# Kernel optimization log

Measured on AMD Instinct MI355X. Metric: run time of the kernel, lower is better.

Reference implementation:

```python
import jax, jax.numpy as jnp
import numpy as np

TAU = 0.07
COS_EPS = 1e-8   # torch F.cosine_similarity eps
L1_EPS = 1e-12   # torch F.normalize eps
MM_EPS = 1e-8    # min-max renorm eps

B, C, H, W = 64, 256, 32, 32
S, D = 512, 256


def setup_inputs() -> dict:
    key = jax.random.key(0)
    k1, k2, k3, k4 = jax.random.split(key, 4)
    scale = 1.0 / np.sqrt(D)
    return {
        "image_patches": jax.random.normal(k1, (B, C, H, W), dtype=jnp.float32),
        "text_tokens": jax.random.normal(k2, (B, S, D), dtype=jnp.float32),
        "Wv": jax.random.normal(k3, (D, D), dtype=jnp.float32) * scale,
        "bv": jnp.zeros((D,), dtype=jnp.float32),
        "Wt": jax.random.normal(k4, (D, D), dtype=jnp.float32) * scale,
        "bt": jnp.zeros((D,), dtype=jnp.float32),
    }


def _linear(x, Wgt, b):
    return x @ Wgt.T + b


def _l2n(x, axis=-1):
    n = jnp.maximum(jnp.linalg.norm(x, axis=axis, keepdims=True), COS_EPS)
    return x / n


def _sym_ce_diag(sim):
    # sim [..., N, N]; mean of -log_softmax diagonals along both class axes
    lsm_r = jax.nn.log_softmax(sim, axis=-1)
    lsm_c = jax.nn.log_softmax(sim, axis=-2)
    d_r = jnp.diagonal(lsm_r, axis1=-2, axis2=-1)
    d_c = jnp.diagonal(lsm_c, axis1=-2, axis2=-1)
    return 0.5 * (-jnp.mean(d_r) - jnp.mean(d_c))


def reference(image_patches, text_tokens, Wv, bv, Wt, bt):
    b, c, h, w = image_patches.shape
    hw = h * w
    # b c h w -> b (h w) c, then adapters
    patches = image_patches.reshape(b, c, hw).transpose(0, 2, 1)  # [b, hw, c]
    patches = _linear(patches, Wv, bv)          # [b, hw, d]
    tokens = _linear(text_tokens, Wt, bt)       # [b, s, d]

    # global embeddings: mean-pool then adapter (adapter applied twice on vision path)
    g_img = _linear(jnp.mean(patches, axis=1), Wv, bv)  # [b, d]
    g_txt = _linear(jnp.mean(tokens, axis=1), Wt, bt)   # [b, d]

    # global contrastive loss (cosine sim / tau, symmetric CE over batch)
    g_sim = (_l2n(g_img) @ _l2n(g_txt).T) / TAU         # [b, b]
    global_loss = _sym_ce_diag(g_sim)

    # fine-grained alignment
    sim = jnp.einsum('bpd,bsd->bps', patches, tokens)   # [b, hw, s]
    mn = jnp.min(sim, axis=1, keepdims=True)
    mx = jnp.max(sim, axis=1, keepdims=True)
    sim = (sim - mn) / (mx - mn + MM_EPS)
    sigma = 1.0 / hw
    sim = jnp.where(sim < sigma, 0.0, sim)
    # L1 normalize over patch dim (torch F.normalize p=1 dim=1)
    weights = sim / jnp.maximum(jnp.sum(jnp.abs(sim), axis=1, keepdims=True), L1_EPS)
    lgve = jnp.einsum('bps,bpd->bsd', weights, patches)  # [b, s, d]

    # fine-grained contrastive loss: cosine sim between grouped-vision and text tokens
    f_sim = jnp.einsum('bid,bjd->bij', _l2n(lgve), _l2n(tokens)) / TAU  # [b, s, s]
    fine_loss = _sym_ce_diag(f_sim)

    return global_loss + fine_loss
```

## Files before the change

kernel.cpp:

```cpp
#include <hip/hip_runtime.h>
#include <math.h>

#define BB   64
#define HWP  1024
#define SS   512
#define DD   256
#define TAU_INV (1.0f/0.07f)
#define SIGMA   (1.0f/1024.0f)

typedef unsigned short us;
typedef __attribute__((ext_vector_type(8))) short short8v;
typedef __attribute__((ext_vector_type(8))) unsigned short ushort8v;
typedef __attribute__((ext_vector_type(4))) float floatx4;

__device__ __forceinline__ float bf2f(us u) {
    return __uint_as_float((unsigned)u << 16);
}
__device__ __forceinline__ us f2bf(float f) {
    unsigned u = __float_as_uint(f);
    u += 0x7FFFu + ((u >> 16) & 1u);
    return (us)(u >> 16);
}
__device__ __forceinline__ void split_bf(float v, us& h, us& l) {
    h = f2bf(v);
    l = f2bf(v - bf2f(h));
}

__global__ void zero_out_k(float* out) { if (threadIdx.x == 0) out[0] = 0.0f; }

enum { OPM_F32_ROW = 0, OPM_F32_COL = 1, OPM_SPL_ROW = 2, OPM_SPL_COL = 3,
       OPM_B16_COL = 4, OPM_B16_ROW = 5, OPM_WGT_COL = 6 };
enum { OUT_F32 = 0, OUT_B16 = 1 };

#define LDSTRIDE 40

template<int MODE, int ROWS, int NW>
struct SRegs {
    static constexpr int RR = ROWS / 128;
    static constexpr bool ISF32 = (MODE == OPM_F32_ROW) || (MODE == OPM_F32_COL);
    ushort8v h[ISF32 ? 1 : RR][2];
    ushort8v l[(MODE == OPM_SPL_ROW) ? RR : 1][2];
    float4   f[ISF32 ? RR : 1][4];
};

template<int MODE, int ROWS, int NW>
__device__ __forceinline__ void stage_load(
    const char* p0, const char* p1, int ld, int row0, int k0, int tid,
    SRegs<MODE, ROWS, NW>& R)
{
    #pragma unroll
    for (int rr = 0; rr < ROWS / 128; ++rr) {
        if constexpr (MODE == OPM_SPL_ROW) {
            const us* ph = (const us*)p0;
            const us* pl = (const us*)p1;
            const int i = rr * 128 + (tid >> 1), ko = (tid & 1) * 16;
            const long long g = (long long)(row0 + i) * ld + k0 + ko;
            R.h[rr][0] = *(const ushort8v*)&ph[g];
            R.h[rr][1] = *(const ushort8v*)&ph[g + 8];
            R.l[rr][0] = *(const ushort8v*)&pl[g];
            R.l[rr][1] = *(const ushort8v*)&pl[g + 8];
        } else if constexpr (MODE == OPM_B16_ROW) {
            const us* ph = (const us*)p0;
            if constexpr (NW == 4) {
                const int i = rr * 128 + (tid >> 1), ko = (tid & 1) * 16;
                const long long g = (long long)(row0 + i) * ld + k0 + ko;
                R.h[rr][0] = *(const ushort8v*)&ph[g];
                R.h[rr][1] = *(const ushort8v*)&ph[g + 8];
            } else {
                const int i = rr * 128 + (tid >> 2), ko = (tid & 3) * 8;
                const long long g = (long long)(row0 + i) * ld + k0 + ko;
                R.h[rr][0] = *(const ushort8v*)&ph[g];
            }
        } else if constexpr (MODE == OPM_F32_ROW) {
            const float* pf = (const float*)p0;
            const int i = rr * 128 + (tid >> 1), ko = (tid & 1) * 16;
            const long long g = (long long)(row0 + i) * ld + k0 + ko;
            #pragma unroll
            for (int c = 0; c < 4; ++c)
                R.f[rr][c] = *(const float4*)&pf[g + c * 4];
        } else if constexpr (MODE == OPM_F32_COL) {
            const float* pf = (const float*)p0;
            const int m = rr * 128 + (tid & 127), kh = (tid >> 7) * 16;
            const long long base = (long long)(k0 + kh) * ld + row0 + m;
            #pragma unroll
            for (int c = 0; c < 4; ++c) {
                float4 v;
                v.x = pf[base + (long long)(c * 4 + 0) * ld];
                v.y = pf[base + (long long)(c * 4 + 1) * ld];
                v.z = pf[base + (long long)(c * 4 + 2) * ld];
                v.w = pf[base + (long long)(c * 4 + 3) * ld];
                R.f[rr][c] = v;
            }
        } else {
            const us* ph = (const us*)p0;
            if constexpr (NW == 4) {
                const int m = rr * 128 + (tid & 127), kh = (tid >> 7) * 16;
                const long long base = (long long)(k0 + kh) * ld + row0 + m;
                #pragma unroll
                for (int kk = 0; kk < 8; ++kk) {
                    R.h[rr][0][kk] = ph[base + (long long)kk * ld];
                    R.h[rr][1][kk] = ph[base + (long long)(kk + 8) * ld];
                }
            } else {
                const int m = rr * 128 + (tid & 127), kh = (tid >> 7) * 8;
                const long long base = (long long)(k0 + kh) * ld + row0 + m;
                #pragma unroll
                for (int kk = 0; kk < 8; ++kk)
                    R.h[rr][0][kk] = ph[base + (long long)kk * ld];
            }
        }
    }
}

template<int MODE, int ROWS, int NW>
__device__ __forceinline__ void stage_store(
    const SRegs<MODE, ROWS, NW>& R, us* ldsH, us* ldsL, int tid, float nlo, float inv)
{
    #pragma unroll
    for (int rr = 0; rr < ROWS / 128; ++rr) {
        if constexpr (MODE == OPM_SPL_ROW) {
            const int i = rr * 128 + (tid >> 1), ko = (tid & 1) * 16;
            *(ushort8v*)&ldsH[i * LDSTRIDE + ko]     = R.h[rr][0];
            *(ushort8v*)&ldsH[i * LDSTRIDE + ko + 8] = R.h[rr][1];
            *(ushort8v*)&ldsL[i * LDSTRIDE + ko]     = R.l[rr][0];
            *(ushort8v*)&ldsL[i * LDSTRIDE + ko + 8] = R.l[rr][1];
        } else if constexpr (MODE == OPM_B16_ROW) {
            if constexpr (NW == 4) {
                const int i = rr * 128 + (tid >> 1), ko = (tid & 1) * 16;
                *(ushort8v*)&ldsH[i * LDSTRIDE + ko]     = R.h[rr][0];
                *(ushort8v*)&ldsH[i * LDSTRIDE + ko + 8] = R.h[rr][1];
            } else {
                const int i = rr * 128 + (tid >> 2), ko = (tid & 3) * 8;
                *(ushort8v*)&ldsH[i * LDSTRIDE + ko] = R.h[rr][0];
            }
        } else if constexpr (MODE == OPM_F32_ROW) {
            const int i = rr * 128 + (tid >> 1), ko = (tid & 1) * 16;
            us h16[16], l16a[16];
            #pragma unroll
            for (int c = 0; c < 4; ++c) {
                float4 v = R.f[rr][c];
                split_bf(v.x, h16[c*4+0], l16a[c*4+0]);
                split_bf(v.y, h16[c*4+1], l16a[c*4+1]);
                split_bf(v.z, h16[c*4+2], l16a[c*4+2]);
                split_bf(v.w, h16[c*4+3], l16a[c*4+3]);
            }
            *(ushort8v*)&ldsH[i * LDSTRIDE + ko]     = *(const ushort8v*)&h16[0];
            *(ushort8v*)&ldsH[i * LDSTRIDE + ko + 8] = *(const ushort8v*)&h16[8];
            *(ushort8v*)&ldsL[i * LDSTRIDE + ko]     = *(const ushort8v*)&l16a[0];
            *(ushort8v*)&ldsL[i * LDSTRIDE + ko + 8] = *(const ushort8v*)&l16a[8];
        } else if constexpr (MODE == OPM_F32_COL) {
            const int m = rr * 128 + (tid & 127), kh = (tid >> 7) * 16;
            us vh[16], vl[16];
            #pragma unroll
            for (int c = 0; c < 4; ++c) {
                float4 v = R.f[rr][c];
                split_bf(v.x, vh[c*4+0], vl[c*4+0]);
                split_bf(v.y, vh[c*4+1], vl[c*4+1]);
                split_bf(v.z, vh[c*4+2], vl[c*4+2]);
                split_bf(v.w, vh[c*4+3], vl[c*4+3]);
            }
            *(ushort8v*)&ldsH[m * LDSTRIDE + kh]     = *(const ushort8v*)&vh[0];
            *(ushort8v*)&ldsH[m * LDSTRIDE + kh + 8] = *(const ushort8v*)&vh[8];
            *(ushort8v*)&ldsL[m * LDSTRIDE + kh]     = *(const ushort8v*)&vl[0];
            *(ushort8v*)&ldsL[m * LDSTRIDE + kh + 8] = *(const ushort8v*)&vl[8];
        } else if constexpr (MODE == OPM_B16_COL) {
            if constexpr (NW == 4) {
                const int m = rr * 128 + (tid & 127), kh = (tid >> 7) * 16;
                *(ushort8v*)&ldsH[m * LDSTRIDE + kh]     = R.h[rr][0];
                *(ushort8v*)&ldsH[m * LDSTRIDE + kh + 8] = R.h[rr][1];
            } else {
                const int m = rr * 128 + (tid & 127), kh = (tid >> 7) * 8;
                *(ushort8v*)&ldsH[m * LDSTRIDE + kh] = R.h[rr][0];
            }
        } else if constexpr (MODE == OPM_WGT_COL) {
            if constexpr (NW == 4) {
                const int m = rr * 128 + (tid & 127), kh = (tid >> 7) * 16;
                us v[16];
                #pragma unroll
                for (int kk = 0; kk < 8; ++kk) {
                    const float w0 = fmaf(bf2f(R.h[rr][0][kk]), inv, nlo);
                    const float w1 = fmaf(bf2f(R.h[rr][1][kk]), inv, nlo);
                    v[kk]     = (w0 < SIGMA) ? (us)0 : f2bf(w0);
                    v[kk + 8] = (w1 < SIGMA) ? (us)0 : f2bf(w1);
                }
                *(ushort8v*)&ldsH[m * LDSTRIDE + kh]     = *(const ushort8v*)&v[0];
                *(ushort8v*)&ldsH[m * LDSTRIDE + kh + 8] = *(const ushort8v*)&v[8];
            } else {
                const int m = rr * 128 + (tid & 127), kh = (tid >> 7) * 8;
                us v[8];
                #pragma unroll
                for (int kk = 0; kk < 8; ++kk) {
                    const float w0 = fmaf(bf2f(R.h[rr][0][kk]), inv, nlo);
                    v[kk] = (w0 < SIGMA) ? (us)0 : f2bf(w0);
                }
                *(ushort8v*)&ldsH[m * LDSTRIDE + kh] = *(const ushort8v*)&v[0];
            }
        }
    }
}

template<int AMODE, int BMODE, int OMODE, int EPI, int NT, int PREF, int NW>
__global__ __launch_bounds__(NW * 64) void mfma_gemm(
    const void* A0, const void* A1, const void* B0, const void* B1, void* C0,
    int M, int N, int K, int lda, int ldb, int ldc,
    long long sA, long long sB, long long sC,
    const float* __restrict__ bias, const float* __restrict__ invm,
    const float* __restrict__ invn, float scale,
    const float* __restrict__ wlo, const float* __restrict__ whi,
    float* __restrict__ aux0, float* __restrict__ aux1,
    float* __restrict__ aux2, float* __restrict__ aux3, float* __restrict__ aux4)
{
    constexpr bool ASPL = (AMODE <= OPM_SPL_COL);
    constexpr bool BSPL = (BMODE <= OPM_SPL_COL);
    constexpr int NF = NT / 16;
    constexpr int MI = 8 / NW;
    constexpr int RPW = 128 / NW;
    __shared__ __align__(16) us Ah[128 * LDSTRIDE];
    __shared__ __align__(16) us Al[ASPL ? 128 * LDSTRIDE : 8];
    __shared__ __align__(16) us Bh[NT * LDSTRIDE];
    __shared__ __align__(16) us Bl[BSPL ? NT * LDSTRIDE : 8];
    __shared__ float redm[(EPI >= 3) ? NW * NT : 1];
    __shared__ float reds[(EPI >= 3) ? NW * NT : 1];

    const int tid = threadIdx.x;
    const int w = tid >> 6, lane = tid & 63;
    const int quad = lane >> 4, l16 = lane & 15;

    int bx = blockIdx.x, by = blockIdx.y, bz = blockIdx.z;
    {
        const int nbx = gridDim.x, nby = gridDim.y, nbz = gridDim.z;
        const int nwg = nbx * nby * nbz;
        if ((nwg & 7) == 0) {
            const int hw = bx + nbx * (by + nby * bz);
            const int cpx = nwg >> 3;
            int wk = (hw & 7) * cpx + (hw >> 3);
            bx = wk % nbx; wk /= nbx;
            by = wk % nby; bz = wk / nby;
        }
    }

    const int m0 = bx * 128, n0 = by * NT;
    const int b = bz;

    const char* Ab0 = (const char*)A0 + (long long)b * sA;
    const char* Ab1 = A1 ? (const char*)A1 + (long long)b * sA : nullptr;
    const char* Bb0 = (const char*)B0 + (long long)b * sB;
    const char* Bb1 = B1 ? (const char*)B1 + (long long)b * sB : nullptr;

    float nloA = 0.f, invA = 0.f;
    if constexpr (AMODE == OPM_WGT_COL) {
        const float* wloA = wlo + (long long)b * M;
        const float* whiA = whi + (long long)b * M;
        const float lo = wloA[m0 + (tid & 127)];
        invA = 1.0f / (whiA[m0 + (tid & 127)] - lo + 1e-8f);
        nloA = -lo * invA;
    }

    SRegs<AMODE, 128, NW> RA0, RA1;
    SRegs<BMODE, NT, NW>  RB0, RB1;
    if constexpr (PREF) {
        stage_load<AMODE, 128, NW>(Ab0, Ab1, lda, m0, 0, tid, RA0);
        stage_load<BMODE, NT, NW>(Bb0, Bb1, ldb, n0, 0, tid, RB0);
        stage_load<AMODE, 128, NW>(Ab0, Ab1, lda, m0, 32, tid, RA1);
        stage_load<BMODE, NT, NW>(Bb0, Bb1, ldb, n0, 32, tid, RB1);
    }

    floatx4 acc[MI][NF];
    #pragma unroll
    for (int mi = 0; mi < MI; ++mi)
        #pragma unroll
        for (int ni = 0; ni < NF; ++ni)
            acc[mi][ni] = (floatx4){0.f, 0.f, 0.f, 0.f};

    auto do_mfma = [&]() {
        short8v ah[MI], al[MI];
        #pragma unroll
        for (int mi = 0; mi < MI; ++mi) {
            const int r = (RPW * w + 16 * mi + l16) * LDSTRIDE + quad * 8;
            ah[mi] = *(const short8v*)&Ah[r];
            if constexpr (ASPL) al[mi] = *(const short8v*)&Al[r];
        }
        #pragma unroll
        for (int ni = 0; ni < NF; ++ni) {
            const int rB = (16 * ni + l16) * LDSTRIDE + quad * 8;
            short8v bh = *(const short8v*)&Bh[rB];
            #pragma unroll
            for (int mi = 0; mi < MI; ++mi)
                acc[mi][ni] = __builtin_amdgcn_mfma_f32_16x16x32_bf16(ah[mi], bh, acc[mi][ni], 0, 0, 0);
            if constexpr (BSPL) {
                short8v bl = *(const short8v*)&Bl[rB];
                #pragma unroll
                for (int mi = 0; mi < MI; ++mi)
                    acc[mi][ni] = __builtin_amdgcn_mfma_f32_16x16x32_bf16(ah[mi], bl, acc[mi][ni], 0, 0, 0);
            }
            if constexpr (ASPL) {
                #pragma unroll
                for (int mi = 0; mi < MI; ++mi)
                    acc[mi][ni] = __builtin_amdgcn_mfma_f32_16x16x32_bf16(al[mi], bh, acc[mi][ni], 0, 0, 0);
            }
        }
    };

#define GEMM_SUBSTEP(RAx, RBx, KCUR, KNEXT)                                    \
    do {                                                                       \
        if constexpr (!PREF) {                                                 \
            stage_load<AMODE, 128, NW>(Ab0, Ab1, lda, m0, (KCUR), tid, RAx);   \
            stage_load<BMODE, NT, NW>(Bb0, Bb1, ldb, n0, (KCUR), tid, RBx);    \
        }                                                                      \
        stage_store<AMODE, 128, NW>(RAx, Ah, Al, tid, nloA, invA);             \
        stage_store<BMODE, NT, NW>(RBx, Bh, Bl, tid, 0.f, 0.f);                \
        if constexpr (PREF) {                                                  \
            asm volatile("s_waitcnt lgkmcnt(0)" ::: "memory");                 \
            __builtin_amdgcn_s_barrier();                                      \
            if ((KNEXT) < K) {                                                 \
                stage_load<AMODE, 128, NW>(Ab0, Ab1, lda, m0, (KNEXT), tid, RAx); \
                stage_load<BMODE, NT, NW>(Bb0, Bb1, ldb, n0, (KNEXT), tid, RBx);  \
            }                                                                  \
        } else {                                                               \
            __syncthreads();                                                   \
        }                                                                      \
        do_mfma();                                                             \
        if constexpr (PREF) {                                                  \
            asm volatile("s_waitcnt lgkmcnt(0)" ::: "memory");                 \
            __builtin_amdgcn_s_barrier();                                      \
        } else {                                                               \
            __syncthreads();                                                   \
        }                                                                      \
    } while (0)

    for (int k0 = 0; k0 < K; k0 += 64) {
        GEMM_SUBSTEP(RA0, RB0, k0, k0 + 64);
        GEMM_SUBSTEP(RA1, RB1, k0 + 32, k0 + 96);
    }
#undef GEMM_SUBSTEP

    if constexpr (EPI != 4) {
        char* Cb0 = (char*)C0 + (long long)b * sC;
        #pragma unroll
        for (int mi = 0; mi < MI; ++mi)
            #pragma unroll
            for (int ni = 0; ni < NF; ++ni)
                #pragma unroll
                for (int r = 0; r < 4; ++r) {
                    const int row = m0 + RPW * w + 16 * mi + quad * 4 + r;
                    const int col = n0 + 16 * ni + l16;
                    float v = acc[mi][ni][r];
                    if constexpr (EPI == 1) v += bias[col];
                    const long long idx = (long long)row * ldc + col;
                    if constexpr (OMODE == OUT_F32) ((float*)Cb0)[idx] = v;
                    else                            ((us*)Cb0)[idx] = f2bf(v);
                }
    }

    if constexpr (EPI == 3) {
        #pragma unroll
        for (int ni = 0; ni < NF; ++ni) {
            float lo = 1e30f, hi = -1e30f;
            #pragma unroll
            for (int mi = 0; mi < MI; ++mi)
                #pragma unroll
                for (int r = 0; r < 4; ++r) {
                    const float vr = bf2f(f2bf(acc[mi][ni][r]));
                    lo = fminf(lo, vr); hi = fmaxf(hi, vr);
                }
            lo = fminf(lo, __shfl_xor(lo, 16)); lo = fminf(lo, __shfl_xor(lo, 32));
            hi = fmaxf(hi, __shfl_xor(hi, 16)); hi = fmaxf(hi, __shfl_xor(hi, 32));
            if (quad == 0) {
                redm[w * NT + 16 * ni + l16] = lo;
                reds[w * NT + 16 * ni + l16] = hi;
            }
        }
        __syncthreads();
        if (tid < NT) {
            float lo = 1e30f, hi = -1e30f;
            #pragma unroll
            for (int w4 = 0; w4 < NW; ++w4) {
                lo = fminf(lo, redm[w4 * NT + tid]);
                hi = fmaxf(hi, reds[w4 * NT + tid]);
            }
            const long long o = ((long long)b * N + n0 + tid) * 8 + bx;
            aux0[o] = lo; aux1[o] = hi;
        }
    }

    if constexpr (EPI == 4) {
        float bn[NF];
        #pragma unroll
        for (int ni = 0; ni < NF; ++ni)
            bn[ni] = invn[(long long)b * N + n0 + 16 * ni + l16] * scale;
        float amv[MI * 4];
        #pragma unroll
        for (int mi = 0; mi < MI; ++mi)
            #pragma unroll
            for (int r = 0; r < 4; ++r)
                amv[mi * 4 + r] = invm[(long long)b * M + m0 + RPW * w + 16 * mi + quad * 4 + r];

        #pragma unroll
        for (int mi = 0; mi < MI; ++mi)
            #pragma unroll
            for (int r = 0; r < 4; ++r) {
                const int grow = m0 + RPW * w + 16 * mi + quad * 4 + r;
                float vv[NF];
                float rm = -1e30f;
                #pragma unroll
                for (int ni = 0; ni < NF; ++ni) {
                    const float v = acc[mi][ni][r] * amv[mi * 4 + r] * bn[ni];
                    vv[ni] = v;
                    rm = fmaxf(rm, v);
                    if (grow == n0 + 16 * ni + l16)
                        aux4[(long long)b * M + grow] = v;
                }
                #pragma unroll
                for (int o = 8; o > 0; o >>= 1) rm = fmaxf(rm, __shfl_xor(rm, o));
                float rs = 0.f;
                #pragma unroll
                for (int ni = 0; ni < NF; ++ni) rs += expf(vv[ni] - rm);
                #pragma unroll
                for (int o = 8; o > 0; o >>= 1) rs += __shfl_xor(rs, o);
                if (l16 == 0) {
                    const long long o = ((long long)b * M + grow) * 4 + by;
                    aux0[o] = rm; aux1[o] = rs;
                }
            }

        #pragma unroll
        for (int ni = 0; ni < NF; ++ni) {
            float va[MI * 4];
            float cm = -1e30f;
            #pragma unroll
            for (int mi = 0; mi < MI; ++mi)
                #pragma unroll
                for (int r = 0; r < 4; ++r) {
                    const float v = acc[mi][ni][r] * amv[mi * 4 + r] * bn[ni];
                    va[mi * 4 + r] = v;
                    cm = fmaxf(cm, v);
                }
            cm = fmaxf(cm, __shfl_xor(cm, 16));
            cm = fmaxf(cm, __shfl_xor(cm, 32));
            float cs = 0.f;
            #pragma unroll
            for (int j = 0; j < MI * 4; ++j) cs += expf(va[j] - cm);
            cs += __shfl_xor(cs, 16);
            cs += __shfl_xor(cs, 32);
            if (quad == 0) {
                redm[w * NT + 16 * ni + l16] = cm;
                reds[w * NT + 16 * ni + l16] = cs;
            }
        }
        __syncthreads();
        if (tid < NT) {
            float m = -1e30f, s = 0.f;
            #pragma unroll
            for (int w4 = 0; w4 < NW; ++w4) {
                const float cm = redm[w4 * NT + tid], cs = reds[w4 * NT + tid];
                const float nm = fmaxf(m, cm);
                s = s * expf(m - nm) + cs * expf(cm - nm);
                m = nm;
            }
            const long long o = ((long long)b * N + n0 + tid) * 4 + bx;
            aux2[o] = m; aux3[o] = s;
        }
    }
}


__global__ __launch_bounds__(256) void convert_w_k(
    const float* Wv, const float* Wt, us* Wvh, us* Wvl, us* Wth, us* Wtl)
{
    const int i = blockIdx.x * 256 + threadIdx.x;
    split_bf(Wv[i], Wvh[i], Wvl[i]);
    split_bf(Wt[i], Wth[i], Wtl[i]);
}

__global__ __launch_bounds__(256) void mean_img_k(
    const float* __restrict__ img, float* __restrict__ mimg)
{
    const int row = blockIdx.x * 4 + (threadIdx.x >> 6);
    const int lane = threadIdx.x & 63;
    const float* p = img + (long long)row * 1024;
    float s = 0.f;
    #pragma unroll
    for (int c = 0; c < 4; ++c) {
        float4 v = *(const float4*)&p[(c * 64 + lane) * 4];
        s += v.x + v.y + v.z + v.w;
    }
    #pragma unroll
    for (int o = 32; o > 0; o >>= 1) s += __shfl_xor(s, o);
    if (lane == 0) mimg[row] = s * (1.0f / 1024.0f);
}

__global__ __launch_bounds__(256) void mean_text_s1(
    const float* __restrict__ text, float* __restrict__ part)
{
    const int b = blockIdx.x, ch = blockIdx.y, k = threadIdx.x;
    const float* p = text + ((long long)b * 512 + ch * 64) * 256 + k;
    float s = 0.f;
    for (int r = 0; r < 64; ++r) s += p[r * 256];
    part[(b * 8 + ch) * 256 + k] = s;
}
__global__ __launch_bounds__(256) void mean_text_s2(
    const float* __restrict__ part, float* __restrict__ mt)
{
    const int b = blockIdx.x, k = threadIdx.x;
    float s = 0.f;
    for (int c = 0; c < 8; ++c) s += part[(b * 8 + c) * 256 + k];
    mt[b * 256 + k] = s * (1.0f / 512.0f);
}

__global__ __launch_bounds__(256) void small_adapter_k(
    const float* __restrict__ x, const float* __restrict__ W,
    const float* __restrict__ bias, float* __restrict__ y)
{
    const int b = blockIdx.x, d = threadIdx.x;
    __shared__ float xs[256];
    xs[d] = x[b * 256 + d];
    __syncthreads();
    const float4* w = (const float4*)(W + (long long)d * 256);
    const float4* xv = (const float4*)xs;
    float s = bias[d];
    #pragma unroll 8
    for (int k = 0; k < 64; ++k) {
        const float4 a = xv[k], ww = w[k];
        s += a.x * ww.x + a.y * ww.y + a.z * ww.z + a.w * ww.w;
    }
    y[b * 256 + d] = s;
}


__global__ __launch_bounds__(256) void inv_norm_f32_k(
    const float* __restrict__ x, float* __restrict__ inv)
{
    const int row = blockIdx.x * 4 + (threadIdx.x >> 6);
    const int lane = threadIdx.x & 63;
    float4 v = *(const float4*)&x[(long long)row * 256 + lane * 4];
    float s = v.x * v.x + v.y * v.y + v.z * v.z + v.w * v.w;
    #pragma unroll
    for (int o = 32; o > 0; o >>= 1) s += __shfl_xor(s, o);
    if (lane == 0) inv[row] = 1.0f / fmaxf(sqrtf(s), 1e-8f);
}

__global__ __launch_bounds__(256) void g_sim_k(
    const float* __restrict__ gi, const float* __restrict__ gt,
    const float* __restrict__ invI, const float* __restrict__ invT,
    float* __restrict__ gs)
{
    const int i = blockIdx.x, t = threadIdx.x;
    const int j = t >> 2, part = t & 3;
    __shared__ float a[256];
    a[t] = gi[i * 256 + t];
    __syncthreads();
    const float* bp = gt + (long long)j * 256 + part * 64;
    const float* ap = a + part * 64;
    float s = 0.f;
    #pragma unroll 16
    for (int k = 0; k < 64; ++k) s += ap[k] * bp[k];
    s += __shfl_xor(s, 1);
    s += __shfl_xor(s, 2);
    if (part == 0) gs[i * 64 + j] = s * invI[i] * invT[j] * TAU_INV;
}

__global__ __launch_bounds__(64) void g_lse_k(
    const float* __restrict__ gs, float* __restrict__ out)
{
    const int b = blockIdx.x, lane = threadIdx.x;
    const bool is_col = b >= 64;
    const int r = is_col ? b - 64 : b;
    const float v = is_col ? gs[lane * 64 + r] : gs[r * 64 + lane];
    float m = v;
    #pragma unroll
    for (int o = 32; o > 0; o >>= 1) m = fmaxf(m, __shfl_xor(m, o));
    float s = expf(v - m);
    #pragma unroll
    for (int o = 32; o > 0; o >>= 1) s += __shfl_xor(s, o);
    if (lane == 0)
        atomicAdd(out, ((m + logf(s)) - gs[r * 64 + r]) * (0.5f / 64.0f));
}

__global__ __launch_bounds__(256) void inv_norm_b16_k(
    const us* __restrict__ x, float* __restrict__ inv)
{
    const int row = blockIdx.x * 4 + (threadIdx.x >> 6);
    const int lane = threadIdx.x & 63;
    ushort4 h = *(const ushort4*)&x[(long long)row * 256 + lane * 4];
    const float x0 = bf2f(h.x), x1 = bf2f(h.y), x2 = bf2f(h.z), x3 = bf2f(h.w);
    float s = x0 * x0 + x1 * x1 + x2 * x2 + x3 * x3;
    #pragma unroll
    for (int o = 32; o > 0; o >>= 1) s += __shfl_xor(s, o);
    if (lane == 0) inv[row] = 1.0f / fmaxf(sqrtf(s), 1e-8f);
}


__global__ __launch_bounds__(256) void minmax_merge_k(
    const float* __restrict__ mnp, const float* __restrict__ mxp,
    float* __restrict__ mn, float* __restrict__ mx)
{
    const int idx = blockIdx.x * 256 + threadIdx.x;
    float lo = 1e30f, hi = -1e30f;
    #pragma unroll
    for (int c = 0; c < 8; ++c) {
        lo = fminf(lo, mnp[(long long)idx * 8 + c]);
        hi = fmaxf(hi, mxp[(long long)idx * 8 + c]);
    }
    mn[idx] = lo; mx[idx] = hi;
}

__global__ __launch_bounds__(256) void fine_merge4_k(
    const float* __restrict__ pm, const float* __restrict__ ps,
    const float* __restrict__ diag, float* __restrict__ out)
{
    const int idx = blockIdx.x * 256 + threadIdx.x;
    float m = -1e30f, s = 0.f;
    #pragma unroll
    for (int c = 0; c < 4; ++c) {
        const float cm = pm[(long long)idx * 4 + c], cs = ps[(long long)idx * 4 + c];
        const float nm = fmaxf(m, cm);
        s = s * expf(m - nm) + cs * expf(cm - nm);
        m = nm;
    }
    const float contrib = (m + logf(s)) - diag[idx];
    __shared__ float red[256];
    red[threadIdx.x] = contrib;
    __syncthreads();
    for (int w = 128; w > 0; w >>= 1) {
        if (threadIdx.x < w) red[threadIdx.x] += red[threadIdx.x + w];
        __syncthreads();
    }
    if (threadIdx.x == 0) atomicAdd(out, red[0] * (0.5f / (64.0f * 512.0f)));
}

extern "C" void kernel_launch(void* const* d_in, const int* in_sizes, int n_in,
                              void* d_out, int out_size, void* d_ws, size_t ws_size,
                              hipStream_t stream)
{
    const float* img  = (const float*)d_in[0];
    const float* text = (const float*)d_in[1];
    const float* Wv   = (const float*)d_in[2];
    const float* bv   = (const float*)d_in[3];
    const float* Wt   = (const float*)d_in[4];
    const float* bt   = (const float*)d_in[5];
    float* out = (float*)d_out;
    char* ws = (char*)d_ws;

    us* patches = (us*)(ws + 0);
    us* tokens  = (us*)(ws + 33554432);
    us* simW    = (us*)(ws + 50331648);
    us* lgve    = (us*)(ws + 117440512);
    char* st = ws + 134217728;
    float* mean_img  = (float*)(st + 0);
    float* mean_text = (float*)(st + 65536);
    float* mean_pat  = (float*)(st + 131072);
    float* mean_tok  = (float*)(st + 196608);
    float* g_img     = (float*)(st + 262144);
    float* g_txt     = (float*)(st + 327680);
    float* textpart  = (float*)(st + 393216);
    float* mnp       = (float*)(st + 917504);
    float* mxp       = (float*)(st + 1966080);
    float* mnv       = (float*)(st + 3014656);
    float* mxv       = (float*)(st + 3145728);
    float* inv_l     = (float*)(st + 3276800);
    float* inv_t     = (float*)(st + 3407872);
    us* Wvh = (us*)(st + 3538944);
    us* Wvl = (us*)(st + 3670016);
    us* Wth = (us*)(st + 3801088);
    us* Wtl = (us*)(st + 3932160);
    float* inv_gi  = (float*)(st + 4063232);
    float* inv_gt  = (float*)(st + 4063744);
    float* g_simbf = (float*)(st + 4064256);
    float* pm_row  = (float*)(st + 4194304);
    float* ps_row  = (float*)(st + 4718592);
    float* pm_col  = (float*)(st + 5242880);
    float* ps_col  = (float*)(st + 5767168);
    float* diag    = (float*)(st + 6291456);

    zero_out_k<<<1, 64, 0, stream>>>(out);
    convert_w_k<<<256, 256, 0, stream>>>(Wv, Wt, Wvh, Wvl, Wth, Wtl);

    mean_img_k<<<4096, 256, 0, stream>>>(img, mean_img);
    mean_text_s1<<<dim3(64, 8), 256, 0, stream>>>(text, textpart);
    mean_text_s2<<<64, 256, 0, stream>>>(textpart, mean_text);
    small_adapter_k<<<BB, 256, 0, stream>>>(mean_img, Wv, bv, mean_pat);
    small_adapter_k<<<BB, 256, 0, stream>>>(mean_pat, Wv, bv, g_img);
    small_adapter_k<<<BB, 256, 0, stream>>>(mean_text, Wt, bt, mean_tok);
    small_adapter_k<<<BB, 256, 0, stream>>>(mean_tok, Wt, bt, g_txt);
    inv_norm_f32_k<<<16, 256, 0, stream>>>(g_img, inv_gi);
    inv_norm_f32_k<<<16, 256, 0, stream>>>(g_txt, inv_gt);
    g_sim_k<<<64, 256, 0, stream>>>(g_img, g_txt, inv_gi, inv_gt, g_simbf);
    g_lse_k<<<128, 64, 0, stream>>>(g_simbf, out);

    mfma_gemm<OPM_F32_COL, OPM_SPL_ROW, OUT_B16, 1, 256, 0, 4><<<dim3(8, 1, BB), 256, 0, stream>>>(
        img, nullptr, Wvh, Wvl, patches,
        1024, 256, 256, 1024, 256, 256,
        1048576LL, 0LL, 524288LL, bv, nullptr, nullptr, 0.f, nullptr, nullptr,
        nullptr, nullptr, nullptr, nullptr, nullptr);

    mfma_gemm<OPM_F32_ROW, OPM_SPL_ROW, OUT_B16, 1, 256, 0, 4><<<dim3(4, 1, BB), 256, 0, stream>>>(
        text, nullptr, Wth, Wtl, tokens,
        512, 256, 256, 256, 256, 256,
        524288LL, 0LL, 262144LL, bt, nullptr, nullptr, 0.f, nullptr, nullptr,
        nullptr, nullptr, nullptr, nullptr, nullptr);

    mfma_gemm<OPM_B16_ROW, OPM_B16_ROW, OUT_B16, 3, 128, 1, 4><<<dim3(8, 4, BB), 256, 0, stream>>>(
        patches, nullptr, tokens, nullptr, simW,
        1024, 512, 256, 256, 256, 512,
        524288LL, 262144LL, 1048576LL, nullptr, nullptr, nullptr, 0.f, nullptr, nullptr,
        mnp, mxp, nullptr, nullptr, nullptr);

    minmax_merge_k<<<128, 256, 0, stream>>>(mnp, mxp, mnv, mxv);

    mfma_gemm<OPM_WGT_COL, OPM_B16_COL, OUT_B16, 0, 128, 1, 8><<<dim3(4, 2, BB), 512, 0, stream>>>(
        simW, nullptr, patches, nullptr, lgve,
        512, 256, 1024, 512, 256, 256,
        1048576LL, 524288LL, 262144LL, nullptr, nullptr, nullptr, 0.f, mnv, mxv,
        nullptr, nullptr, nullptr, nullptr, nullptr);

    inv_norm_b16_k<<<8192, 256, 0, stream>>>(lgve, inv_l);
    inv_norm_b16_k<<<8192, 256, 0, stream>>>(tokens, inv_t);

    mfma_gemm<OPM_B16_ROW, OPM_B16_ROW, OUT_B16, 4, 128, 1, 8><<<dim3(4, 4, BB), 512, 0, stream>>>(
        lgve, nullptr, tokens, nullptr, nullptr,
        512, 512, 256, 256, 256, 512,
        262144LL, 262144LL, 0LL, nullptr, inv_l, inv_t, TAU_INV, nullptr, nullptr,
        pm_row, ps_row, pm_col, ps_col, diag);

    fine_merge4_k<<<128, 256, 0, stream>>>(pm_row, ps_row, diag, out);
    fine_merge4_k<<<128, 256, 0, stream>>>(pm_col, ps_col, diag, out);
}
```

Before: 388.3 us.

## Use direct global-to-LDS DMA loads and transpose the similarity matrix layout

Adds a global_load_lds DMA path with a double-buffered LDS pipeline for the pure-bf16 GEMMs (the similarity GEMM and the fine-loss GEMM). This removes the register staging round trip. The similarity GEMM now computes tokens x patches, so the sim matrix is stored transposed [s, hw]. That lets the min/max reduction use in-wavefront shuffles over rows, and lets the weighted-sum GEMM read weights row-major instead of with strided column loads. The cost is an unpadded 32-wide LDS layout that may cause bank conflicts, plus only one MFMA row tile per wave in the DMA path.

```diff
diff --git a/kernel.cpp b/kernel.cpp
--- a/kernel.cpp
+++ b/kernel.cpp
@@ -26,10 +26,16 @@
     l = f2bf(v - bf2f(h));
 }
 
+__device__ __forceinline__ void dma16(const us* g, us* l) {
+    __builtin_amdgcn_global_load_lds(
+        (const __attribute__((address_space(1))) unsigned int*)g,
+        (__attribute__((address_space(3))) unsigned int*)l, 16, 0, 0);
+}
+
 __global__ void zero_out_k(float* out) { if (threadIdx.x == 0) out[0] = 0.0f; }
 
 enum { OPM_F32_ROW = 0, OPM_F32_COL = 1, OPM_SPL_ROW = 2, OPM_SPL_COL = 3,
-       OPM_B16_COL = 4, OPM_B16_ROW = 5, OPM_WGT_COL = 6 };
+       OPM_B16_COL = 4, OPM_B16_ROW = 5, OPM_WGT_COL = 6, OPM_WGT_ROW = 7 };
 enum { OUT_F32 = 0, OUT_B16 = 1 };
 
 #define LDSTRIDE 40
@@ -59,7 +65,7 @@
             R.h[rr][1] = *(const ushort8v*)&ph[g + 8];
             R.l[rr][0] = *(const ushort8v*)&pl[g];
             R.l[rr][1] = *(const ushort8v*)&pl[g + 8];
-        } else if constexpr (MODE == OPM_B16_ROW) {
+        } else if constexpr (MODE == OPM_B16_ROW || MODE == OPM_WGT_ROW) {
             const us* ph = (const us*)p0;
             if constexpr (NW == 4) {
                 const int i = rr * 128 + (tid >> 1), ko = (tid & 1) * 16;
@@ -91,7 +97,7 @@
                 v.w = pf[base + (long long)(c * 4 + 3) * ld];
                 R.f[rr][c] = v;
             }
-        } else {
+        } else if constexpr (MODE == OPM_B16_COL) {
             const us* ph = (const us*)p0;
             if constexpr (NW == 4) {
                 const int m = rr * 128 + (tid & 127), kh = (tid >> 7) * 16;
@@ -133,6 +139,15 @@
                 const int i = rr * 128 + (tid >> 2), ko = (tid & 3) * 8;
                 *(ushort8v*)&ldsH[i * LDSTRIDE + ko] = R.h[rr][0];
             }
+        } else if constexpr (MODE == OPM_WGT_ROW) {
+            const int i = tid >> 2, ko = (tid & 3) * 8;
+            us v[8];
+            #pragma unroll
+            for (int j = 0; j < 8; ++j) {
+                const float w0 = fmaf(bf2f(R.h[0][0][j]), inv, nlo);
+                v[j] = (w0 < SIGMA) ? (us)0 : f2bf(w0);
+            }
+            *(ushort8v*)&ldsH[i * LDSTRIDE + ko] = *(const ushort8v*)&v[0];
         } else if constexpr (MODE == OPM_F32_ROW) {
             const int i = rr * 128 + (tid >> 1), ko = (tid & 1) * 16;
             us h16[16], l16a[16];
@@ -166,40 +181,21 @@
         } else if constexpr (MODE == OPM_B16_COL) {
             if constexpr (NW == 4) {
                 const int m = rr * 128 + (tid & 127), kh = (tid >> 7) * 16;
-                *(ushort8v*)&ldsH[m * LDSTRIDE + kh]     = R.h[rr][0];
-                *(ushort8v*)&ldsH[m * LDSTRIDE + kh + 8] = R.h[rr][1];
-            } else {
-                const int m = rr * 128 + (tid & 127), kh = (tid >> 7) * 8;
-                *(ushort8v*)&ldsH[m * LDSTRIDE + kh] = R.h[rr][0];
-            }
-        } else if constexpr (MODE == OPM_WGT_COL) {
-            if constexpr (NW == 4) {
-                const int m = rr * 128 + (tid & 127), kh = (tid >> 7) * 16;
                 us v[16];
                 #pragma unroll
-                for (int kk = 0; kk < 8; ++kk) {
-                    const float w0 = fmaf(bf2f(R.h[rr][0][kk]), inv, nlo);
-                    const float w1 = fmaf(bf2f(R.h[rr][1][kk]), inv, nlo);
-                    v[kk]     = (w0 < SIGMA) ? (us)0 : f2bf(w0);
-                    v[kk + 8] = (w1 < SIGMA) ? (us)0 : f2bf(w1);
-                }
+                for (int kk = 0; kk < 16; ++kk)
+                    v[kk] = (kk < 8) ? R.h[rr][0][kk & 7] : R.h[rr][1][kk & 7];
                 *(ushort8v*)&ldsH[m * LDSTRIDE + kh]     = *(const ushort8v*)&v[0];
                 *(ushort8v*)&ldsH[m * LDSTRIDE + kh + 8] = *(const ushort8v*)&v[8];
             } else {
                 const int m = rr * 128 + (tid & 127), kh = (tid >> 7) * 8;
-                us v[8];
-                #pragma unroll
-                for (int kk = 0; kk < 8; ++kk) {
-                    const float w0 = fmaf(bf2f(R.h[rr][0][kk]), inv, nlo);
-                    v[kk] = (w0 < SIGMA) ? (us)0 : f2bf(w0);
-                }
-                *(ushort8v*)&ldsH[m * LDSTRIDE + kh] = *(const ushort8v*)&v[0];
-            }
-        }
-    }
-}
-
-template<int AMODE, int BMODE, int OMODE, int EPI, int NT, int PREF, int NW>
+                *(ushort8v*)&ldsH[m * LDSTRIDE + kh] = R.h[rr][0];
+            }
+        }
+    }
+}
+
+template<int AMODE, int BMODE, int OMODE, int EPI, int NT, int PREF, int NW, int DMA>
 __global__ __launch_bounds__(NW * 64) void mfma_gemm(
     const void* A0, const void* A1, const void* B0, const void* B1, void* C0,
     int M, int N, int K, int lda, int ldb, int ldc,
@@ -215,12 +211,14 @@
     constexpr int NF = NT / 16;
     constexpr int MI = 8 / NW;
     constexpr int RPW = 128 / NW;
-    __shared__ __align__(16) us Ah[128 * LDSTRIDE];
-    __shared__ __align__(16) us Al[ASPL ? 128 * LDSTRIDE : 8];
-    __shared__ __align__(16) us Bh[NT * LDSTRIDE];
-    __shared__ __align__(16) us Bl[BSPL ? NT * LDSTRIDE : 8];
-    __shared__ float redm[(EPI >= 3) ? NW * NT : 1];
-    __shared__ float reds[(EPI >= 3) ? NW * NT : 1];
+    __shared__ __align__(16) us Ah[DMA ? 8 : 128 * LDSTRIDE];
+    __shared__ __align__(16) us Al[(!DMA && ASPL) ? 128 * LDSTRIDE : 8];
+    __shared__ __align__(16) us Bh[DMA ? 8 : NT * LDSTRIDE];
+    __shared__ __align__(16) us Bl[(!DMA && BSPL) ? NT * LDSTRIDE : 8];
+    __shared__ __align__(16) us AhD[DMA ? 2 * 128 * 32 : 8];
+    __shared__ __align__(16) us BhD[DMA ? 2 * NT * 32 : 8];
+    __shared__ float redm[(EPI == 4) ? NW * NT : 1];
+    __shared__ float reds[(EPI == 4) ? NW * NT : 1];
 
     const int tid = threadIdx.x;
     const int w = tid >> 6, lane = tid & 63;
@@ -247,24 +245,6 @@
     const char* Bb0 = (const char*)B0 + (long long)b * sB;
     const char* Bb1 = B1 ? (const char*)B1 + (long long)b * sB : nullptr;
 
-    float nloA = 0.f, invA = 0.f;
-    if constexpr (AMODE == OPM_WGT_COL) {
-        const float* wloA = wlo + (long long)b * M;
-        const float* whiA = whi + (long long)b * M;
-        const float lo = wloA[m0 + (tid & 127)];
-        invA = 1.0f / (whiA[m0 + (tid & 127)] - lo + 1e-8f);
-        nloA = -lo * invA;
-    }
-
-    SRegs<AMODE, 128, NW> RA0, RA1;
-    SRegs<BMODE, NT, NW>  RB0, RB1;
-    if constexpr (PREF) {
-        stage_load<AMODE, 128, NW>(Ab0, Ab1, lda, m0, 0, tid, RA0);
-        stage_load<BMODE, NT, NW>(Bb0, Bb1, ldb, n0, 0, tid, RB0);
-        stage_load<AMODE, 128, NW>(Ab0, Ab1, lda, m0, 32, tid, RA1);
-        stage_load<BMODE, NT, NW>(Bb0, Bb1, ldb, n0, 32, tid, RB1);
-    }
-
     floatx4 acc[MI][NF];
     #pragma unroll
     for (int mi = 0; mi < MI; ++mi)
@@ -272,34 +252,97 @@
         for (int ni = 0; ni < NF; ++ni)
             acc[mi][ni] = (floatx4){0.f, 0.f, 0.f, 0.f};
 
-    auto do_mfma = [&]() {
-        short8v ah[MI], al[MI];
-        #pragma unroll
-        for (int mi = 0; mi < MI; ++mi) {
-            const int r = (RPW * w + 16 * mi + l16) * LDSTRIDE + quad * 8;
-            ah[mi] = *(const short8v*)&Ah[r];
-            if constexpr (ASPL) al[mi] = *(const short8v*)&Al[r];
-        }
-        #pragma unroll
-        for (int ni = 0; ni < NF; ++ni) {
-            const int rB = (16 * ni + l16) * LDSTRIDE + quad * 8;
-            short8v bh = *(const short8v*)&Bh[rB];
-            #pragma unroll
-            for (int mi = 0; mi < MI; ++mi)
-                acc[mi][ni] = __builtin_amdgcn_mfma_f32_16x16x32_bf16(ah[mi], bh, acc[mi][ni], 0, 0, 0);
-            if constexpr (BSPL) {
-                short8v bl = *(const short8v*)&Bl[rB];
+    if constexpr (DMA) {
+        const us* Abu = (const us*)Ab0;
+        const us* Bbu = (const us*)Bb0;
+        const int drow = 16 * w + (lane >> 2);
+        const int dcol = (lane & 3) * 8;
+        const us* aS = Abu + (long long)(m0 + drow) * lda + dcol;
+        const us* bS = Bbu + (long long)(n0 + drow) * ldb + dcol;
+        us* aD = &AhD[0] + 512 * w;
+        us* bD = &BhD[0] + 512 * w;
+        const int NTL = K >> 5;
+
+        dma16(aS,      aD);
+        dma16(bS,      bD);
+        dma16(aS + 32, aD + 128 * 32);
+        dma16(bS + 32, bD + NT * 32);
+
+        int cur = 0;
+        for (int t = 0; t < NTL; ++t) {
+            if (t + 1 == NTL) asm volatile("s_waitcnt vmcnt(0)" ::: "memory");
+            else              asm volatile("s_waitcnt vmcnt(2)" ::: "memory");
+            __builtin_amdgcn_s_barrier();
+            asm volatile("" ::: "memory");
+
+            {
+                const us* Ac = &AhD[cur * 128 * 32];
+                const us* Bc = &BhD[cur * NT * 32];
+                short8v ah = *(const short8v*)&Ac[(16 * w + l16) * 32 + quad * 8];
+                #pragma unroll
+                for (int ni = 0; ni < NF; ++ni) {
+                    short8v bh = *(const short8v*)&Bc[(16 * ni + l16) * 32 + quad * 8];
+                    acc[0][ni] = __builtin_amdgcn_mfma_f32_16x16x32_bf16(ah, bh, acc[0][ni], 0, 0, 0);
+                }
+            }
+
+            asm volatile("" ::: "memory");
+            __builtin_amdgcn_s_barrier();
+            if (t + 2 < NTL) {
+                const long long off = (long long)(t + 2) * 32;
+                dma16(aS + off, aD + cur * 128 * 32);
+                dma16(bS + off, bD + cur * NT * 32);
+            }
+            cur ^= 1;
+        }
+    } else {
+        float nloA = 0.f, invA = 0.f;
+        if constexpr (AMODE == OPM_WGT_ROW) {
+            const float* wloA = wlo + (long long)b * M;
+            const float* whiA = whi + (long long)b * M;
+            const int row = m0 + (tid >> 2);
+            const float lo = wloA[row];
+            invA = 1.0f / (whiA[row] - lo + 1e-8f);
+            nloA = -lo * invA;
+        }
+
+        SRegs<AMODE, 128, NW> RA0, RA1;
+        SRegs<BMODE, NT, NW>  RB0, RB1;
+        if constexpr (PREF) {
+            stage_load<AMODE, 128, NW>(Ab0, Ab1, lda, m0, 0, tid, RA0);
+            stage_load<BMODE, NT, NW>(Bb0, Bb1, ldb, n0, 0, tid, RB0);
+            stage_load<AMODE, 128, NW>(Ab0, Ab1, lda, m0, 32, tid, RA1);
+            stage_load<BMODE, NT, NW>(Bb0, Bb1, ldb, n0, 32, tid, RB1);
+        }
+
+        auto do_mfma = [&]() {
+            short8v ah[MI], al[MI];
+            #pragma unroll
+            for (int mi = 0; mi < MI; ++mi) {
+                const int r = (RPW * w + 16 * mi + l16) * LDSTRIDE + quad * 8;
+                ah[mi] = *(const short8v*)&Ah[r];
+                if constexpr (ASPL) al[mi] = *(const short8v*)&Al[r];
+            }
+            #pragma unroll
+            for (int ni = 0; ni < NF; ++ni) {
+                const int rB = (16 * ni + l16) * LDSTRIDE + quad * 8;
+                short8v bh = *(const short8v*)&Bh[rB];
                 #pragma unroll
                 for (int mi = 0; mi < MI; ++mi)
-                    acc[mi][ni] = __builtin_amdgcn_mfma_f32_16x16x32_bf16(ah[mi], bl, acc[mi][ni], 0, 0, 0);
-            }
-            if constexpr (ASPL) {
-                #pragma unroll
-                for (int mi = 0; mi < MI; ++mi)
-                    acc[mi][ni] = __builtin_amdgcn_mfma_f32_16x16x32_bf16(al[mi], bh, acc[mi][ni], 0, 0, 0);
-            }
-        }
-    };
+                    acc[mi][ni] = __builtin_amdgcn_mfma_f32_16x16x32_bf16(ah[mi], bh, acc[mi][ni], 0, 0, 0);
+                if constexpr (BSPL) {
+                    short8v bl = *(const short8v*)&Bl[rB];
+                    #pragma unroll
+                    for (int mi = 0; mi < MI; ++mi)
+                        acc[mi][ni] = __builtin_amdgcn_mfma_f32_16x16x32_bf16(ah[mi], bl, acc[mi][ni], 0, 0, 0);
+                }
+                if constexpr (ASPL) {
+                    #pragma unroll
+                    for (int mi = 0; mi < MI; ++mi)
+                        acc[mi][ni] = __builtin_amdgcn_mfma_f32_16x16x32_bf16(al[mi], bh, acc[mi][ni], 0, 0, 0);
+                }
+            }
+        };
 
 #define GEMM_SUBSTEP(RAx, RBx, KCUR, KNEXT)                                    \
     do {                                                                       \
@@ -328,11 +371,12 @@
         }                                                                      \
     } while (0)
 
-    for (int k0 = 0; k0 < K; k0 += 64) {
-        GEMM_SUBSTEP(RA0, RB0, k0, k0 + 64);
-        GEMM_SUBSTEP(RA1, RB1, k0 + 32, k0 + 96);
-    }
+        for (int k0 = 0; k0 < K; k0 += 64) {
+            GEMM_SUBSTEP(RA0, RB0, k0, k0 + 64);
+            GEMM_SUBSTEP(RA1, RB1, k0 + 32, k0 + 96);
+        }
 #undef GEMM_SUBSTEP
+    }
 
     if constexpr (EPI != 4) {
         char* Cb0 = (char*)C0 + (long long)b * sC;
@@ -354,32 +398,22 @@
 
     if constexpr (EPI == 3) {
         #pragma unroll
-        for (int ni = 0; ni < NF; ++ni) {
+        for (int r = 0; r < 4; ++r) {
+            const int grow = m0 + RPW * w + quad * 4 + r;
             float lo = 1e30f, hi = -1e30f;
             #pragma unroll
-            for (int mi = 0; mi < MI; ++mi)
-                #pragma unroll
-                for (int r = 0; r < 4; ++r) {
-                    const float vr = bf2f(f2bf(acc[mi][ni][r]));
-                    lo = fminf(lo, vr); hi = fmaxf(hi, vr);
-                }
-            lo = fminf(lo, __shfl_xor(lo, 16)); lo = fminf(lo, __shfl_xor(lo, 32));
-            hi = fmaxf(hi, __shfl_xor(hi, 16)); hi = fmaxf(hi, __shfl_xor(hi, 32));
-            if (quad == 0) {
-                redm[w * NT + 16 * ni + l16] = lo;
-                reds[w * NT + 16 * ni + l16] = hi;
-            }
-        }
-        __syncthreads();
-        if (tid < NT) {
-            float lo = 1e30f, hi = -1e30f;
-            #pragma unroll
-            for (int w4 = 0; w4 < NW; ++w4) {
-                lo = fminf(lo, redm[w4 * NT + tid]);
-                hi = fmaxf(hi, reds[w4 * NT + tid]);
-            }
-            const long long o = ((long long)b * N + n0 + tid) * 8 + bx;
-            aux0[o] = lo; aux1[o] = hi;
+            for (int ni = 0; ni < NF; ++ni) {
+                const float vr = bf2f(f2bf(acc[0][ni][r]));
+                lo = fminf(lo, vr); hi = fmaxf(hi, vr);
+            }
+            lo = fminf(lo, __shfl_xor(lo, 1)); hi = fmaxf(hi, __shfl_xor(hi, 1));
+            lo = fminf(lo, __shfl_xor(lo, 2)); hi = fmaxf(hi, __shfl_xor(hi, 2));
+            lo = fminf(lo, __shfl_xor(lo, 4)); hi = fmaxf(hi, __shfl_xor(hi, 4));
+            lo = fminf(lo, __shfl_xor(lo, 8)); hi = fmaxf(hi, __shfl_xor(hi, 8));
+            if (l16 == 0) {
+                const long long o = ((long long)b * M + grow) * 8 + by;
+                aux0[o] = lo; aux1[o] = hi;
+            }
         }
     }
 
@@ -643,7 +677,7 @@
 
     us* patches = (us*)(ws + 0);
     us* tokens  = (us*)(ws + 33554432);
-    us* simW    = (us*)(ws + 50331648);
+    us* simT    = (us*)(ws + 50331648);
     us* lgve    = (us*)(ws + 117440512);
     char* st = ws + 134217728;
     float* mean_img  = (float*)(st + 0);
@@ -687,36 +721,36 @@
     g_sim_k<<<64, 256, 0, stream>>>(g_img, g_txt, inv_gi, inv_gt, g_simbf);
     g_lse_k<<<128, 64, 0, stream>>>(g_simbf, out);
 
-    mfma_gemm<OPM_F32_COL, OPM_SPL_ROW, OUT_B16, 1, 256, 0, 4><<<dim3(8, 1, BB), 256, 0, stream>>>(
+    mfma_gemm<OPM_F32_COL, OPM_SPL_ROW, OUT_B16, 1, 256, 0, 4, 0><<<dim3(8, 1, BB), 256, 0, stream>>>(
         img, nullptr, Wvh, Wvl, patches,
         1024, 256, 256, 1024, 256, 256,
         1048576LL, 0LL, 524288LL, bv, nullptr, nullptr, 0.f, nullptr, nullptr,
         nullptr, nullptr, nullptr, nullptr, nullptr);
 
-    mfma_gemm<OPM_F32_ROW, OPM_SPL_ROW, OUT_B16, 1, 256, 0, 4><<<dim3(4, 1, BB), 256, 0, stream>>>(
+    mfma_gemm<OPM_F32_ROW, OPM_SPL_ROW, OUT_B16, 1, 256, 0, 4, 0><<<dim3(4, 1, BB), 256, 0, stream>>>(
         text, nullptr, Wth, Wtl, tokens,
         512, 256, 256, 256, 256, 256,
         524288LL, 0LL, 262144LL, bt, nullptr, nullptr, 0.f, nullptr, nullptr,
         nullptr, nullptr, nullptr, nullptr, nullptr);
 
-    mfma_gemm<OPM_B16_ROW, OPM_B16_ROW, OUT_B16, 3, 128, 1, 4><<<dim3(8, 4, BB), 256, 0, stream>>>(
-        patches, nullptr, tokens, nullptr, simW,
-        1024, 512, 256, 256, 256, 512,
-        524288LL, 262144LL, 1048576LL, nullptr, nullptr, nullptr, 0.f, nullptr, nullptr,
+    mfma_gemm<OPM_B16_ROW, OPM_B16_ROW, OUT_B16, 3, 128, 0, 8, 1><<<dim3(4, 8, BB), 512, 0, stream>>>(
+        tokens, nullptr, patches, nullptr, simT,
+        512, 1024, 256, 256, 256, 1024,
+        262144LL, 524288LL, 1048576LL, nullptr, nullptr, nullptr, 0.f, nullptr, nullptr,
         mnp, mxp, nullptr, nullptr, nullptr);
 
     minmax_merge_k<<<128, 256, 0, stream>>>(mnp, mxp, mnv, mxv);
 
-    mfma_gemm<OPM_WGT_COL, OPM_B16_COL, OUT_B16, 0, 128, 1, 8><<<dim3(4, 2, BB), 512, 0, stream>>>(
-        simW, nullptr, patches, nullptr, lgve,
-        512, 256, 1024, 512, 256, 256,
+    mfma_gemm<OPM_WGT_ROW, OPM_B16_COL, OUT_B16, 0, 128, 1, 8, 0><<<dim3(4, 2, BB), 512, 0, stream>>>(
+        simT, nullptr, patches, nullptr, lgve,
+        512, 256, 1024, 1024, 256, 256,
         1048576LL, 524288LL, 262144LL, nullptr, nullptr, nullptr, 0.f, mnv, mxv,
         nullptr, nullptr, nullptr, nullptr, nullptr);
 
     inv_norm_b16_k<<<8192, 256, 0, stream>>>(lgve, inv_l);
     inv_norm_b16_k<<<8192, 256, 0, stream>>>(tokens, inv_t);
 
-    mfma_gemm<OPM_B16_ROW, OPM_B16_ROW, OUT_B16, 4, 128, 1, 8><<<dim3(4, 4, BB), 512, 0, stream>>>(
+    mfma_gemm<OPM_B16_ROW, OPM_B16_ROW, OUT_B16, 4, 128, 0, 8, 1><<<dim3(4, 4, BB), 512, 0, stream>>>(
         lgve, nullptr, tokens, nullptr, nullptr,
         512, 512, 256, 256, 256, 512,
         262144LL, 262144LL, 0LL, nullptr, inv_l, inv_t, TAU_INV, nullptr, nullptr,
```

Result: no change. 395.5 us (+1.8%).
